# Optimization experiments

Hardware: AMD Instinct MI355X
Metric: run time of the kernel (lower is better)

The kernel has to match this reference:

```python
import jax, jax.numpy as jnp
import numpy as np
import math

N_GRAPHS = 25
NODES_PER = 2000
N = N_GRAPHS * NODES_PER      # 50000 total nodes
E = 800000                    # total edges
D = 128                       # hidden = out_dim
VOCAB = 30                    # node_len
NLAYERS = 4                   # gcn_num_layers


def setup_inputs() -> dict:
    key = jax.random.key(0)
    ks = jax.random.split(key, 16)
    labels = jax.random.randint(ks[0], (N,), 0, VOCAB)
    src = jax.random.randint(ks[1], (E,), 0, N)
    dst = jax.random.randint(ks[2], (E,), 0, N)
    # true permutations per graph (as the torch code assumes)
    perms = jax.vmap(lambda k: jax.random.permutation(k, NODES_PER))(
        jax.random.split(ks[3], N_GRAPHS))
    s = 0.02
    emb = jax.random.normal(ks[4], (VOCAB, D)) * s
    Ws = jax.random.normal(ks[5], (NLAYERS, D, D)) * s
    bs = jnp.zeros((NLAYERS, D))
    # MLPReadout(D, D) with L=2: D -> D//2 -> D//4 -> D
    w1 = jax.random.normal(ks[6], (D, D // 2)) * s
    b1 = jnp.zeros((D // 2,))
    w2 = jax.random.normal(ks[7], (D // 2, D // 4)) * s
    b2 = jnp.zeros((D // 4,))
    w3 = jax.random.normal(ks[8], (D // 4, D)) * s
    b3 = jnp.zeros((D,))
    return {"labels": labels, "src": src, "dst": dst, "perms": perms,
            "emb": emb, "Ws": Ws, "bs": bs,
            "w1": w1, "b1": b1, "w2": w2, "b2": b2, "w3": w3, "b3": b3}


def _pos_encoding(perms):
    # sinusoidal table [NODES_PER, D]; position starts at 1 per the torch code
    pos = (jnp.arange(NODES_PER, dtype=jnp.float32) + 1.0)[:, None]       # [n,1]
    div = jnp.exp(jnp.arange(0, D, 2, dtype=jnp.float32)
                  * (-math.log(10000.0) / D))                              # [D/2]
    ang = pos * div                                                        # [n,D/2]
    table = jnp.stack([jnp.sin(ang), jnp.cos(ang)], axis=-1).reshape(NODES_PER, D)
    # pes[i][perm_i] = table  (scatter rows per graph)
    pe = jax.vmap(lambda p: jnp.zeros((NODES_PER, D), jnp.float32).at[p].set(table))(perms)
    return pe.reshape(N, D)


def reference(labels, src, dst, perms, emb, Ws, bs, w1, b1, w2, b2, w3, b3):
    h = emb[labels]                                   # embedding lookup [N,D]
    h = h + _pos_encoding(perms)

    ones = jnp.ones((E,), jnp.float32)
    deg_out = jnp.maximum(jax.ops.segment_sum(ones, src, num_segments=N), 1.0)
    deg_in = jnp.maximum(jax.ops.segment_sum(ones, dst, num_segments=N), 1.0)
    isq_src = deg_out ** -0.5                         # DGL GraphConv norm='both'
    isq_dst = deg_in ** -0.5

    for l in range(NLAYERS):
        hn = h * isq_src[:, None]
        m = jax.ops.segment_sum(hn[src], dst, num_segments=N)  # gather-scatter
        m = m * isq_dst[:, None]
        out = jax.nn.relu(m @ Ws[l] + bs[l])
        h = out + h                                   # residual (all dims equal)

    # MLPReadout: D -> D//2 -> D//4 -> D
    x = jax.nn.relu(h @ w1 + b1)
    x = jax.nn.relu(x @ w2 + b2)
    return x @ w3 + b3                                # [N, D]
```

## Files before the change

### kernel.cpp

```cpp
#include <hip/hip_runtime.h>

#define N_NODES 50000
#define N_EDGES 800000
#define D 128
#define NLAYERS 4
#define NODES_PER 2000
#define CAP 64

__device__ inline unsigned rne16(float f) {
    unsigned u = __float_as_uint(f);
    return (u + 0x7fffu + ((u >> 16) & 1u)) >> 16;
}
__device__ inline unsigned pack_bf2(float a, float b) {
    return rne16(a) | (rne16(b) << 16);
}
__device__ inline float4 bf4_to_f4(uint2 v) {
    float4 r;
    r.x = __uint_as_float(v.x << 16);
    r.y = __uint_as_float(v.x & 0xffff0000u);
    r.z = __uint_as_float(v.y << 16);
    r.w = __uint_as_float(v.y & 0xffff0000u);
    return r;
}

__global__ void build_kernel(const int* __restrict__ src, const int* __restrict__ dst,
                             int* __restrict__ cursor, int* __restrict__ cnt_out_rep,
                             int* __restrict__ bucket) {
    int e = blockIdx.x * 256 + threadIdx.x;
    if (e < N_EDGES) {
        int s = src[e], d = dst[e];
        atomicAdd(&cnt_out_rep[(blockIdx.x & 3) * N_NODES + s], 1);
        int pos = atomicAdd(&cursor[d], 1);
        if (pos < CAP) bucket[d * CAP + pos] = s;
    }
}

__global__ void finalize_kernel(const int* __restrict__ cursor,
                                const int* __restrict__ cnt_out_rep,
                                float* __restrict__ isq_src, float* __restrict__ isq_dst) {
    int i = blockIdx.x * 256 + threadIdx.x;
    if (i < N_NODES) {
        int co = cnt_out_rep[i] + cnt_out_rep[N_NODES + i] +
                 cnt_out_rep[2 * N_NODES + i] + cnt_out_rep[3 * N_NODES + i];
        isq_src[i] = rsqrtf((float)max(co, 1));
        isq_dst[i] = rsqrtf((float)max(cursor[i], 1));
    }
}

__global__ void init_h_kernel(const int* __restrict__ labels, const int* __restrict__ perms,
                              const float* __restrict__ emb, const float* __restrict__ isq_src,
                              float* __restrict__ h, unsigned short* __restrict__ hs16) {
    int b = blockIdx.x;
    int g = b / NODES_PER;
    int i = b - g * NODES_PER;
    int node = g * NODES_PER + perms[b];
    int d = threadIdx.x;
    int k = d >> 1;
    float ang = (float)(i + 1) * expf((float)(2 * k) * (-9.210340371976184f / 128.0f));
    float pe = (d & 1) ? cosf(ang) : sinf(ang);
    float v = emb[labels[node] * D + d] + pe;
    h[node * D + d] = v;
    hs16[node * D + d] = (unsigned short)rne16(v * isq_src[node]);
}

__global__ __launch_bounds__(256) void aggregate_kernel(const unsigned short* __restrict__ hs16,
        const int* __restrict__ cursor, const int* __restrict__ bucket,
        const float* __restrict__ isq_dst, unsigned short* __restrict__ m16) {
    int node = blockIdx.x * 4 + (threadIdx.x >> 6);
    int lane = threadIdx.x & 63;
    int q = lane >> 4;
    int col = lane & 15;
    int deg = min(cursor[node], CAP);
    int start = node * CAP;
    int end = start + deg;
    const unsigned short* hb = hs16 + col * 8;
    float a[8] = {0.f, 0.f, 0.f, 0.f, 0.f, 0.f, 0.f, 0.f};

    int e = start;
    for (; e + 8 <= end; e += 8) {
        int s0 = bucket[e + q];
        int s1 = bucket[e + 4 + q];
        uint4 v0 = *(const uint4*)&hb[s0 * D];
        uint4 v1 = *(const uint4*)&hb[s1 * D];
        float4 f0 = bf4_to_f4(make_uint2(v0.x, v0.y));
        float4 f1 = bf4_to_f4(make_uint2(v0.z, v0.w));
        float4 f2 = bf4_to_f4(make_uint2(v1.x, v1.y));
        float4 f3 = bf4_to_f4(make_uint2(v1.z, v1.w));
        a[0] += f0.x; a[1] += f0.y; a[2] += f0.z; a[3] += f0.w;
        a[4] += f1.x; a[5] += f1.y; a[6] += f1.z; a[7] += f1.w;
        a[0] += f2.x; a[1] += f2.y; a[2] += f2.z; a[3] += f2.w;
        a[4] += f3.x; a[5] += f3.y; a[6] += f3.z; a[7] += f3.w;
    }
    if (e + 4 <= end) {
        int s0 = bucket[e + q];
        uint4 v0 = *(const uint4*)&hb[s0 * D];
        float4 f0 = bf4_to_f4(make_uint2(v0.x, v0.y));
        float4 f1 = bf4_to_f4(make_uint2(v0.z, v0.w));
        a[0] += f0.x; a[1] += f0.y; a[2] += f0.z; a[3] += f0.w;
        a[4] += f1.x; a[5] += f1.y; a[6] += f1.z; a[7] += f1.w;
        e += 4;
    }
    int r = end - e;
    if (q < r) {
        int s0 = bucket[e + q];
        uint4 v0 = *(const uint4*)&hb[s0 * D];
        float4 f0 = bf4_to_f4(make_uint2(v0.x, v0.y));
        float4 f1 = bf4_to_f4(make_uint2(v0.z, v0.w));
        a[0] += f0.x; a[1] += f0.y; a[2] += f0.z; a[3] += f0.w;
        a[4] += f1.x; a[5] += f1.y; a[6] += f1.z; a[7] += f1.w;
    }
#pragma unroll
    for (int i = 0; i < 8; ++i) {
        a[i] += __shfl_xor(a[i], 16, 64);
        a[i] += __shfl_xor(a[i], 32, 64);
    }
    if (q == 0) {
        float wd = isq_dst[node];
        uint4 o;
        o.x = pack_bf2(a[0] * wd, a[1] * wd);
        o.y = pack_bf2(a[2] * wd, a[3] * wd);
        o.z = pack_bf2(a[4] * wd, a[5] * wd);
        o.w = pack_bf2(a[6] * wd, a[7] * wd);
        *(uint4*)&m16[node * D + col * 8] = o;
    }
}

__global__ __launch_bounds__(256) void layer_kernel(const unsigned short* __restrict__ m16,
                                                    const float* __restrict__ W,
                                                    const float* __restrict__ bias,
                                                    float* __restrict__ h,
                                                    unsigned short* __restrict__ hs16,
                                                    const float* __restrict__ isq) {
    __shared__ float msT[128][68];
    int t = threadIdx.x;
    int rowbase = blockIdx.x * 64;

    for (int i = t; i < 2048; i += 256) {
        int row = i >> 5;
        int kc = i & 31;
        int grow = rowbase + row;
        float4 v = make_float4(0.f, 0.f, 0.f, 0.f);
        if (grow < N_NODES) v = bf4_to_f4(*(const uint2*)&m16[grow * D + kc * 4]);
        int cs = row ^ ((kc & 7) << 2);
        msT[kc * 4 + 0][cs] = v.x;
        msT[kc * 4 + 1][cs] = v.y;
        msT[kc * 4 + 2][cs] = v.z;
        msT[kc * 4 + 3][cs] = v.w;
    }
    __syncthreads();

    int tx = t & 15, ty = t >> 4;
    int c0 = tx * 8;
    int r0 = ty * 4;
    float acc[4][8];
    float4 bv0 = *(const float4*)&bias[c0];
    float4 bv1 = *(const float4*)&bias[c0 + 4];
#pragma unroll
    for (int i = 0; i < 4; ++i) {
        acc[i][0] = bv0.x; acc[i][1] = bv0.y; acc[i][2] = bv0.z; acc[i][3] = bv0.w;
        acc[i][4] = bv1.x; acc[i][5] = bv1.y; acc[i][6] = bv1.z; acc[i][7] = bv1.w;
    }
#pragma unroll 4
    for (int k = 0; k < 128; ++k) {
        int s4 = ((k >> 2) & 7) << 2;
        float4 wa = *(const float4*)&W[k * D + c0];
        float4 wb = *(const float4*)&W[k * D + c0 + 4];
        float4 ma = *(const float4*)&msT[k][r0 ^ s4];
        float mv[4] = {ma.x, ma.y, ma.z, ma.w};
        float wv[8] = {wa.x, wa.y, wa.z, wa.w, wb.x, wb.y, wb.z, wb.w};
#pragma unroll
        for (int i = 0; i < 4; ++i)
#pragma unroll
            for (int j = 0; j < 8; ++j)
                acc[i][j] += mv[i] * wv[j];
    }
#pragma unroll
    for (int i = 0; i < 4; ++i) {
        int row = rowbase + r0 + i;
        if (row < N_NODES) {
            float4 h0 = *(const float4*)&h[row * D + c0];
            float4 h1 = *(const float4*)&h[row * D + c0 + 4];
            float4 o0, o1;
            o0.x = fmaxf(acc[i][0], 0.f) + h0.x;
            o0.y = fmaxf(acc[i][1], 0.f) + h0.y;
            o0.z = fmaxf(acc[i][2], 0.f) + h0.z;
            o0.w = fmaxf(acc[i][3], 0.f) + h0.w;
            o1.x = fmaxf(acc[i][4], 0.f) + h1.x;
            o1.y = fmaxf(acc[i][5], 0.f) + h1.y;
            o1.z = fmaxf(acc[i][6], 0.f) + h1.z;
            o1.w = fmaxf(acc[i][7], 0.f) + h1.w;
            *(float4*)&h[row * D + c0] = o0;
            *(float4*)&h[row * D + c0 + 4] = o1;
            if (isq) {
                float s = isq[row];
                uint4 p;
                p.x = pack_bf2(o0.x * s, o0.y * s);
                p.y = pack_bf2(o0.z * s, o0.w * s);
                p.z = pack_bf2(o1.x * s, o1.y * s);
                p.w = pack_bf2(o1.z * s, o1.w * s);
                *(uint4*)&hs16[row * D + c0] = p;
            }
        }
    }
}

__global__ __launch_bounds__(256, 4) void readout_kernel(const float* __restrict__ h,
        const float* __restrict__ w1, const float* __restrict__ b1,
        const float* __restrict__ w2, const float* __restrict__ b2,
        const float* __restrict__ w3, const float* __restrict__ b3,
        float* __restrict__ out) {
    __shared__ float hT[128][68];
    int t = threadIdx.x;
    int rowbase = blockIdx.x * 64;
    int tx = t & 15, ty = t >> 4;
    int r0 = ty * 4;

    for (int i = t; i < 2048; i += 256) {
        int row = i >> 5;
        int kc = i & 31;
        int grow = rowbase + row;
        float4 v = (grow < N_NODES) ? *(const float4*)&h[grow * D + kc * 4]
                                    : make_float4(0.f, 0.f, 0.f, 0.f);
        int cs = row ^ ((kc & 7) << 2);
        hT[kc * 4 + 0][cs] = v.x;
        hT[kc * 4 + 1][cs] = v.y;
        hT[kc * 4 + 2][cs] = v.z;
        hT[kc * 4 + 3][cs] = v.w;
    }
    __syncthreads();

    float a1[4][4];
    {
        int c1 = tx * 4;
        float4 bv = *(const float4*)&b1[c1];
#pragma unroll
        for (int i = 0; i < 4; ++i) {
            a1[i][0] = bv.x; a1[i][1] = bv.y; a1[i][2] = bv.z; a1[i][3] = bv.w;
        }
#pragma unroll 2
        for (int k = 0; k < 128; ++k) {
            int s4 = ((k >> 2) & 7) << 2;
            float4 ma = *(const float4*)&hT[k][r0 ^ s4];
            float4 wv = *(const float4*)&w1[k * 64 + c1];
            float mv[4] = {ma.x, ma.y, ma.z, ma.w};
#pragma unroll
            for (int i = 0; i < 4; ++i) {
                a1[i][0] += mv[i] * wv.x;
                a1[i][1] += mv[i] * wv.y;
                a1[i][2] += mv[i] * wv.z;
                a1[i][3] += mv[i] * wv.w;
            }
        }
    }
    __syncthreads();
    {
        int c1 = tx * 4;
#pragma unroll
        for (int j = 0; j < 4; ++j) {
            int c = c1 + j;
            int cs = r0 ^ (((c >> 2) & 7) << 2);
            *(float4*)&hT[c][cs] = make_float4(fmaxf(a1[0][j], 0.f), fmaxf(a1[1][j], 0.f),
                                               fmaxf(a1[2][j], 0.f), fmaxf(a1[3][j], 0.f));
        }
    }
    __syncthreads();

    {
        int c2 = tx * 2;
        float a2[4][2];
        float2 bv = *(const float2*)&b2[c2];
#pragma unroll
        for (int i = 0; i < 4; ++i) { a2[i][0] = bv.x; a2[i][1] = bv.y; }
#pragma unroll 2
        for (int k = 0; k < 64; ++k) {
            int s4 = ((k >> 2) & 7) << 2;
            float4 ma = *(const float4*)&hT[k][r0 ^ s4];
            float2 wv = *(const float2*)&w2[k * 32 + c2];
            float mv[4] = {ma.x, ma.y, ma.z, ma.w};
#pragma unroll
            for (int i = 0; i < 4; ++i) {
                a2[i][0] += mv[i] * wv.x;
                a2[i][1] += mv[i] * wv.y;
            }
        }
#pragma unroll
        for (int j = 0; j < 2; ++j) {
            int c = c2 + j;
            int cs = r0 ^ (((c >> 2) & 7) << 2);
            *(float4*)&hT[64 + c][cs] = make_float4(fmaxf(a2[0][j], 0.f), fmaxf(a2[1][j], 0.f),
                                                    fmaxf(a2[2][j], 0.f), fmaxf(a2[3][j], 0.f));
        }
    }
    __syncthreads();

    {
        int c0 = tx * 8;
        float acc[4][8];
        float4 bv0 = *(const float4*)&b3[c0];
        float4 bv1 = *(const float4*)&b3[c0 + 4];
#pragma unroll
        for (int i = 0; i < 4; ++i) {
            acc[i][0] = bv0.x; acc[i][1] = bv0.y; acc[i][2] = bv0.z; acc[i][3] = bv0.w;
            acc[i][4] = bv1.x; acc[i][5] = bv1.y; acc[i][6] = bv1.z; acc[i][7] = bv1.w;
        }
#pragma unroll 4
        for (int k = 0; k < 32; ++k) {
            int s4 = ((k >> 2) & 7) << 2;
            float4 ma = *(const float4*)&hT[64 + k][r0 ^ s4];
            float4 wa = *(const float4*)&w3[k * D + c0];
            float4 wb = *(const float4*)&w3[k * D + c0 + 4];
            float mv[4] = {ma.x, ma.y, ma.z, ma.w};
            float wv[8] = {wa.x, wa.y, wa.z, wa.w, wb.x, wb.y, wb.z, wb.w};
#pragma unroll
            for (int i = 0; i < 4; ++i)
#pragma unroll
                for (int j = 0; j < 8; ++j)
                    acc[i][j] += mv[i] * wv[j];
        }
#pragma unroll
        for (int i = 0; i < 4; ++i) {
            int row = rowbase + r0 + i;
            if (row < N_NODES) {
                *(float4*)&out[row * D + c0] =
                    make_float4(acc[i][0], acc[i][1], acc[i][2], acc[i][3]);
                *(float4*)&out[row * D + c0 + 4] =
                    make_float4(acc[i][4], acc[i][5], acc[i][6], acc[i][7]);
            }
        }
    }
}

extern "C" void kernel_launch(void* const* d_in, const int* in_sizes, int n_in,
                              void* d_out, int out_size, void* d_ws, size_t ws_size,
                              hipStream_t stream) {
    const int*   labels = (const int*)d_in[0];
    const int*   src    = (const int*)d_in[1];
    const int*   dst    = (const int*)d_in[2];
    const int*   perms  = (const int*)d_in[3];
    const float* emb    = (const float*)d_in[4];
    const float* Ws     = (const float*)d_in[5];
    const float* bs     = (const float*)d_in[6];
    const float* w1     = (const float*)d_in[7];
    const float* b1     = (const float*)d_in[8];
    const float* w2     = (const float*)d_in[9];
    const float* b2     = (const float*)d_in[10];
    const float* w3     = (const float*)d_in[11];
    const float* b3     = (const float*)d_in[12];
    float* out = (float*)d_out;

    char* p = (char*)d_ws;
    auto alloc = [&](size_t bytes) -> char* {
        char* r = p;
        p += (bytes + 255) & ~size_t(255);
        return r;
    };
    float*          h       = (float*)alloc((size_t)N_NODES * D * 4);
    unsigned short* hs16    = (unsigned short*)alloc((size_t)N_NODES * D * 2);
    unsigned short* m16     = (unsigned short*)alloc((size_t)N_NODES * D * 2);
    float*          isq_src = (float*)alloc((size_t)N_NODES * 4);
    float*          isq_dst = (float*)alloc((size_t)N_NODES * 4);
    int*            cursor  = (int*)alloc((size_t)5 * N_NODES * 4);
    int*            cnt_rep = cursor + N_NODES;
    int*            bucket  = (int*)alloc((size_t)N_NODES * CAP * 4);

    hipMemsetAsync(cursor, 0, (size_t)5 * N_NODES * 4, stream);
    build_kernel<<<(N_EDGES + 255) / 256, 256, 0, stream>>>(src, dst, cursor, cnt_rep, bucket);
    finalize_kernel<<<(N_NODES + 255) / 256, 256, 0, stream>>>(cursor, cnt_rep,
                                                               isq_src, isq_dst);
    init_h_kernel<<<N_NODES, 128, 0, stream>>>(labels, perms, emb, isq_src, h, hs16);

    for (int l = 0; l < NLAYERS; ++l) {
        aggregate_kernel<<<N_NODES / 4, 256, 0, stream>>>(hs16, cursor, bucket, isq_dst, m16);
        layer_kernel<<<(N_NODES + 63) / 64, 256, 0, stream>>>(
            m16, Ws + (size_t)l * D * D, bs + (size_t)l * D, h, hs16,
            (l < NLAYERS - 1) ? isq_src : (const float*)nullptr);
    }
    readout_kernel<<<(N_NODES + 63) / 64, 256, 0, stream>>>(h, w1, b1, w2, b2, w3, b3, out);
}
```

Before: 515.2 us.

## Replace FP32 layer GEMM with bf16 MFMA kernel and shrink edge buckets

Rewrites the per-layer dense transform to use 16x16x32 bf16 MFMA instructions. A pre-transposed bf16 copy of the weights is built once, and A fragments are loaded directly from the bf16 aggregated messages, replacing the shared-memory FP32 FMA tile. Edge bucket source indices are also stored as 16-bit values, halving that gather-index traffic. Rounding the weights to bf16 lowers precision, and the epilogue now does scalar per-element stores.

```diff
diff --git a/kernel.cpp b/kernel.cpp
--- a/kernel.cpp
+++ b/kernel.cpp
@@ -6,6 +6,9 @@
 #define NLAYERS 4
 #define NODES_PER 2000
 #define CAP 64
+
+typedef __attribute__((ext_vector_type(8))) short bf16x8;
+typedef __attribute__((ext_vector_type(4))) float f32x4;
 
 __device__ inline unsigned rne16(float f) {
     unsigned u = __float_as_uint(f);
@@ -25,13 +28,13 @@
 
 __global__ void build_kernel(const int* __restrict__ src, const int* __restrict__ dst,
                              int* __restrict__ cursor, int* __restrict__ cnt_out_rep,
-                             int* __restrict__ bucket) {
+                             unsigned short* __restrict__ bucket) {
     int e = blockIdx.x * 256 + threadIdx.x;
     if (e < N_EDGES) {
         int s = src[e], d = dst[e];
         atomicAdd(&cnt_out_rep[(blockIdx.x & 3) * N_NODES + s], 1);
         int pos = atomicAdd(&cursor[d], 1);
-        if (pos < CAP) bucket[d * CAP + pos] = s;
+        if (pos < CAP) bucket[d * CAP + pos] = (unsigned short)s;
     }
 }
 
@@ -44,6 +47,17 @@
                  cnt_out_rep[2 * N_NODES + i] + cnt_out_rep[3 * N_NODES + i];
         isq_src[i] = rsqrtf((float)max(co, 1));
         isq_dst[i] = rsqrtf((float)max(cursor[i], 1));
+    }
+}
+
+__global__ void transpose_w_kernel(const float* __restrict__ Ws,
+                                   unsigned short* __restrict__ Wt) {
+    int l = blockIdx.x;
+    const float* W = Ws + (size_t)l * D * D;
+    unsigned short* T = Wt + (size_t)l * D * D;
+    for (int i = threadIdx.x; i < D * D; i += 256) {
+        int k = i >> 7, n = i & 127;
+        T[n * D + k] = (unsigned short)rne16(W[i]);
     }
 }
 
@@ -64,7 +78,7 @@
 }
 
 __global__ __launch_bounds__(256) void aggregate_kernel(const unsigned short* __restrict__ hs16,
-        const int* __restrict__ cursor, const int* __restrict__ bucket,
+        const int* __restrict__ cursor, const unsigned short* __restrict__ bucket,
         const float* __restrict__ isq_dst, unsigned short* __restrict__ m16) {
     int node = blockIdx.x * 4 + (threadIdx.x >> 6);
     int lane = threadIdx.x & 63;
@@ -125,80 +139,42 @@
     }
 }
 
-__global__ __launch_bounds__(256) void layer_kernel(const unsigned short* __restrict__ m16,
-                                                    const float* __restrict__ W,
-                                                    const float* __restrict__ bias,
-                                                    float* __restrict__ h,
-                                                    unsigned short* __restrict__ hs16,
-                                                    const float* __restrict__ isq) {
-    __shared__ float msT[128][68];
-    int t = threadIdx.x;
-    int rowbase = blockIdx.x * 64;
-
-    for (int i = t; i < 2048; i += 256) {
-        int row = i >> 5;
-        int kc = i & 31;
-        int grow = rowbase + row;
-        float4 v = make_float4(0.f, 0.f, 0.f, 0.f);
-        if (grow < N_NODES) v = bf4_to_f4(*(const uint2*)&m16[grow * D + kc * 4]);
-        int cs = row ^ ((kc & 7) << 2);
-        msT[kc * 4 + 0][cs] = v.x;
-        msT[kc * 4 + 1][cs] = v.y;
-        msT[kc * 4 + 2][cs] = v.z;
-        msT[kc * 4 + 3][cs] = v.w;
-    }
-    __syncthreads();
-
-    int tx = t & 15, ty = t >> 4;
-    int c0 = tx * 8;
-    int r0 = ty * 4;
-    float acc[4][8];
-    float4 bv0 = *(const float4*)&bias[c0];
-    float4 bv1 = *(const float4*)&bias[c0 + 4];
-#pragma unroll
-    for (int i = 0; i < 4; ++i) {
-        acc[i][0] = bv0.x; acc[i][1] = bv0.y; acc[i][2] = bv0.z; acc[i][3] = bv0.w;
-        acc[i][4] = bv1.x; acc[i][5] = bv1.y; acc[i][6] = bv1.z; acc[i][7] = bv1.w;
-    }
-#pragma unroll 4
-    for (int k = 0; k < 128; ++k) {
-        int s4 = ((k >> 2) & 7) << 2;
-        float4 wa = *(const float4*)&W[k * D + c0];
-        float4 wb = *(const float4*)&W[k * D + c0 + 4];
-        float4 ma = *(const float4*)&msT[k][r0 ^ s4];
-        float mv[4] = {ma.x, ma.y, ma.z, ma.w};
-        float wv[8] = {wa.x, wa.y, wa.z, wa.w, wb.x, wb.y, wb.z, wb.w};
-#pragma unroll
-        for (int i = 0; i < 4; ++i)
-#pragma unroll
-            for (int j = 0; j < 8; ++j)
-                acc[i][j] += mv[i] * wv[j];
-    }
-#pragma unroll
-    for (int i = 0; i < 4; ++i) {
-        int row = rowbase + r0 + i;
-        if (row < N_NODES) {
-            float4 h0 = *(const float4*)&h[row * D + c0];
-            float4 h1 = *(const float4*)&h[row * D + c0 + 4];
-            float4 o0, o1;
-            o0.x = fmaxf(acc[i][0], 0.f) + h0.x;
-            o0.y = fmaxf(acc[i][1], 0.f) + h0.y;
-            o0.z = fmaxf(acc[i][2], 0.f) + h0.z;
-            o0.w = fmaxf(acc[i][3], 0.f) + h0.w;
-            o1.x = fmaxf(acc[i][4], 0.f) + h1.x;
-            o1.y = fmaxf(acc[i][5], 0.f) + h1.y;
-            o1.z = fmaxf(acc[i][6], 0.f) + h1.z;
-            o1.w = fmaxf(acc[i][7], 0.f) + h1.w;
-            *(float4*)&h[row * D + c0] = o0;
-            *(float4*)&h[row * D + c0 + 4] = o1;
-            if (isq) {
-                float s = isq[row];
-                uint4 p;
-                p.x = pack_bf2(o0.x * s, o0.y * s);
-                p.y = pack_bf2(o0.z * s, o0.w * s);
-                p.z = pack_bf2(o1.x * s, o1.y * s);
-                p.w = pack_bf2(o1.z * s, o1.w * s);
-                *(uint4*)&hs16[row * D + c0] = p;
+__global__ __launch_bounds__(256) void layer_mfma_kernel(const unsigned short* __restrict__ m16,
+        const unsigned short* __restrict__ Wt, const float* __restrict__ bias,
+        float* __restrict__ h, unsigned short* __restrict__ hs16,
+        const float* __restrict__ isq) {
+    int wave = threadIdx.x >> 6;
+    int lane = threadIdx.x & 63;
+    int rowbase = blockIdx.x * 64 + wave * 16;
+    int col16 = lane & 15;
+    int kq8 = (lane >> 4) * 8;
+
+    int arow = min(rowbase + col16, N_NODES - 1);
+    bf16x8 afrag[4];
+#pragma unroll
+    for (int kk = 0; kk < 4; ++kk)
+        afrag[kk] = *(const bf16x8*)&m16[(size_t)arow * D + kk * 32 + kq8];
+
+    int orow0 = rowbase + (lane >> 4) * 4;
+
+#pragma unroll 2
+    for (int nt = 0; nt < 8; ++nt) {
+        int ncol = nt * 16 + col16;
+        float bv = bias[ncol];
+        f32x4 acc = {bv, bv, bv, bv};
+#pragma unroll
+        for (int kk = 0; kk < 4; ++kk) {
+            bf16x8 bfrag = *(const bf16x8*)&Wt[(size_t)ncol * D + kk * 32 + kq8];
+            acc = __builtin_amdgcn_mfma_f32_16x16x32_bf16(afrag[kk], bfrag, acc, 0, 0, 0);
+        }
+#pragma unroll
+        for (int r = 0; r < 4; ++r) {
+            int row = orow0 + r;
+            if (row < N_NODES) {
+                size_t idx = (size_t)row * D + ncol;
+                float o = fmaxf(acc[r], 0.f) + h[idx];
+                h[idx] = o;
+                if (isq) hs16[idx] = (unsigned short)rne16(o * isq[row]);
             }
         }
     }
@@ -357,13 +333,15 @@
     float*          h       = (float*)alloc((size_t)N_NODES * D * 4);
     unsigned short* hs16    = (unsigned short*)alloc((size_t)N_NODES * D * 2);
     unsigned short* m16     = (unsigned short*)alloc((size_t)N_NODES * D * 2);
+    unsigned short* Wt      = (unsigned short*)alloc((size_t)NLAYERS * D * D * 2);
     float*          isq_src = (float*)alloc((size_t)N_NODES * 4);
     float*          isq_dst = (float*)alloc((size_t)N_NODES * 4);
     int*            cursor  = (int*)alloc((size_t)5 * N_NODES * 4);
     int*            cnt_rep = cursor + N_NODES;
-    int*            bucket  = (int*)alloc((size_t)N_NODES * CAP * 4);
+    unsigned short* bucket  = (unsigned short*)alloc((size_t)N_NODES * CAP * 2);
 
     hipMemsetAsync(cursor, 0, (size_t)5 * N_NODES * 4, stream);
+    transpose_w_kernel<<<NLAYERS, 256, 0, stream>>>(Ws, Wt);
     build_kernel<<<(N_EDGES + 255) / 256, 256, 0, stream>>>(src, dst, cursor, cnt_rep, bucket);
     finalize_kernel<<<(N_NODES + 255) / 256, 256, 0, stream>>>(cursor, cnt_rep,
                                                                isq_src, isq_dst);
@@ -371,8 +349,8 @@
 
     for (int l = 0; l < NLAYERS; ++l) {
         aggregate_kernel<<<N_NODES / 4, 256, 0, stream>>>(hs16, cursor, bucket, isq_dst, m16);
-        layer_kernel<<<(N_NODES + 63) / 64, 256, 0, stream>>>(
-            m16, Ws + (size_t)l * D * D, bs + (size_t)l * D, h, hs16,
+        layer_mfma_kernel<<<(N_NODES + 63) / 64, 256, 0, stream>>>(
+            m16, Wt + (size_t)l * D * D, bs + (size_t)l * D, h, hs16,
             (l < NLAYERS - 1) ? isq_src : (const float*)nullptr);
     }
     readout_kernel<<<(N_NODES + 63) / 64, 256, 0, stream>>>(h, w1, b1, w2, b2, w3, b3, out);
```

After: 481.6 us. -6.5%, faster.
